# Optimization experiments

Hardware: AMD Instinct MI355X
Metric: run time of the kernel (lower is better)

## Reference

```python
import jax, jax.numpy as jnp
import numpy as np

TASK_NUM = 100000
WORKER_NUM = 500
FEATURE_SIZE = 512
CLASS_NUM = 10
ANSWER_NUM = 1000000
HIDDEN = 128
NUM_NODES = TASK_NUM + WORKER_NUM


def setup_inputs() -> dict:
    key = jax.random.key(0)
    ks = jax.random.split(key, 10)
    task_ids = jax.random.randint(ks[0], (ANSWER_NUM,), 0, TASK_NUM, dtype=jnp.int32)
    worker_ids = jax.random.randint(ks[1], (ANSWER_NUM,), 0, WORKER_NUM, dtype=jnp.int32)
    label_ids = jax.random.randint(ks[2], (ANSWER_NUM,), 0, CLASS_NUM, dtype=jnp.int32)
    answers = jnp.stack([task_ids, worker_ids, label_ids], axis=1)  # [A,3]
    return {
        "task_feature": jax.random.normal(ks[3], (TASK_NUM, FEATURE_SIZE), jnp.float32),
        "answers": answers,
        "worker_feature": jax.random.normal(ks[4], (WORKER_NUM, HIDDEN), jnp.float32),
        "W_efc": jax.random.normal(ks[5], (FEATURE_SIZE, HIDDEN), jnp.float32) * 0.05,
        "b_efc": jnp.zeros((HIDDEN,), jnp.float32),
        "W_mean": jax.random.normal(ks[6], (HIDDEN, CLASS_NUM), jnp.float32) * 0.05,
        "b_mean": jnp.zeros((CLASS_NUM,), jnp.float32),
        "W_log_std": jax.random.normal(ks[7], (HIDDEN, CLASS_NUM), jnp.float32) * 0.05,
        "b_log_std": jnp.zeros((CLASS_NUM,), jnp.float32),
        "eps": jax.random.normal(ks[8], (NUM_NODES, CLASS_NUM), jnp.float32),
    }


def _gcn_edges(task_ids, worker_ids):
    # Bipartite edges doubled to be symmetric, plus self-loops (renorm trick).
    row0 = task_ids
    col0 = worker_ids + TASK_NUM
    self_idx = jnp.arange(NUM_NODES, dtype=jnp.int32)
    row = jnp.concatenate([row0, col0, self_idx])
    col = jnp.concatenate([col0, row0, self_idx])
    deg = jax.ops.segment_sum(jnp.ones_like(row, dtype=jnp.float32), row,
                              num_segments=NUM_NODES)
    dinv = jax.lax.rsqrt(deg)  # deg >= 1 thanks to self-loops
    w = dinv[row] * dinv[col]  # [E]
    return row, col, w, row0, col0


def _gcn(x, kernel, bias, row, col, w):
    h = x @ kernel                                   # [N, C]
    msg = h[col] * w[:, None]                        # gather + scale
    return jax.ops.segment_sum(msg, row, num_segments=NUM_NODES) + bias


def reference(task_feature, answers, worker_feature, W_efc, b_efc,
              W_mean, b_mean, W_log_std, b_log_std, eps):
    row, col, w, row0, col0 = _gcn_edges(answers[:, 0], answers[:, 1])
    tf_h = jax.nn.relu(task_feature @ W_efc + b_efc)           # [T, 128]
    x = jnp.concatenate([tf_h, worker_feature], axis=0)        # [N, 128]
    mean = _gcn(x, W_mean, b_mean, row, col, w)                # [N, C]
    log_std = _gcn(x, W_log_std, b_log_std, row, col, w)       # [N, C]
    z = mean + (eps * 0.01) * jnp.exp(log_std)                 # reparam, stddev 0.01
    crowd_out = z[row0] * z[col0]                              # [A, C]
    return crowd_out, mean, log_std
```

## Files before the change

kernel.cpp:

```cpp
#include <hip/hip_runtime.h>

#define T_NUM   100000
#define W_NUM   500
#define N_NODES 100500
#define A_NUM   1000000
#define FEAT    512
#define HID     128
#define CLS     10

#define CSR_STRIDE  40
#define CSRT_STRIDE 2432
#define BM          64
#define HPAD        136
#define NRANGE      8
#define TRNG        (T_NUM / NRANGE)
#define WRNG        64
#define CHUNK       2048
#define NCHUNK      ((A_NUM + CHUNK - 1) / CHUNK)
#define BLD_CAP     64

typedef short bf16x8 __attribute__((ext_vector_type(8)));
typedef float f32x4  __attribute__((ext_vector_type(4)));

__device__ __forceinline__ unsigned cvtpk(float lo, float hi) {
    unsigned r;
    asm("v_cvt_pk_bf16_f32 %0, %1, %2" : "=v"(r) : "v"(lo), "v"(hi));
    return r;
}
__device__ __forceinline__ unsigned short f2bf1(float x) {
    return (unsigned short)cvtpk(x, x);
}

__global__ __launch_bounds__(256) void k_build(
        const int* __restrict__ answers, int* __restrict__ cnt,
        int* __restrict__ wcur, int* __restrict__ tick,
        unsigned short* __restrict__ csrW, int* __restrict__ csrT) {
    __shared__ int lcnt[WRNG];
    __shared__ int llist[WRNG * BLD_CAP];
    __shared__ int s_chunk;

    int xcc;
    asm volatile("s_getreg_b32 %0, hwreg(HW_REG_XCC_ID)" : "=s"(xcc));
    const int r   = xcc & (NRANGE - 1);
    const int tlo = r * TRNG, thi = tlo + TRNG;
    const int wlo = r * WRNG;

    for (int i = threadIdx.x; i < WRNG; i += 256) lcnt[i] = 0;

    for (;;) {
        __syncthreads();
        if (threadIdx.x == 0) s_chunk = atomicAdd(&tick[r * 16], 1);
        __syncthreads();
        const int c = s_chunk;
        if (c >= NCHUNK) break;
        const int base = c * CHUNK;
        const int end  = (base + CHUNK < A_NUM) ? base + CHUNK : A_NUM;
        for (int a = base + threadIdx.x; a < end; a += 256) {
            int t = __builtin_nontemporal_load(answers + a * 3);
            int w = __builtin_nontemporal_load(answers + a * 3 + 1);
            if (t >= tlo && t < thi) {
                int p = atomicAdd(&cnt[t], 1);
                if (p < CSR_STRIDE) csrW[(size_t)t * CSR_STRIDE + p] = (unsigned short)w;
            }
            int wr = w - wlo;
            if (wr >= 0 && wr < WRNG && w < W_NUM) {
                int s = atomicAdd(&lcnt[wr], 1);
                if (s < BLD_CAP) llist[wr * BLD_CAP + s] = t;
                else {
                    int q = atomicAdd(&wcur[w * 16], 1);
                    if (q < CSRT_STRIDE) csrT[(size_t)w * CSRT_STRIDE + q] = t;
                }
            }
        }
    }
    __syncthreads();

    for (int wr = threadIdx.x; wr < WRNG; wr += 256) {
        int w = wlo + wr;
        if (w >= W_NUM) continue;
        int c = lcnt[wr];
        if (c > BLD_CAP) c = BLD_CAP;
        if (c == 0) continue;
        int qb = atomicAdd(&wcur[w * 16], c);
        int* dst = csrT + (size_t)w * CSRT_STRIDE;
        for (int j = 0; j < c; j++) {
            int q = qb + j;
            if (q < CSRT_STRIDE) dst[q] = llist[wr * BLD_CAP + j];
        }
    }
}

__global__ void k_prepw(const float* __restrict__ W, unsigned short* __restrict__ Wt,
                        unsigned short* __restrict__ B2t,
                        const float* __restrict__ WF,
                        const float* __restrict__ Wm, const float* __restrict__ Wl,
                        const int* __restrict__ wcur,
                        float* __restrict__ g) {
    int bid = blockIdx.x;
    if (bid < HID) {
        int c = bid;
        for (int k = threadIdx.x; k < FEAT; k += blockDim.x)
            Wt[(size_t)c * FEAT + k] = f2bf1(W[(size_t)k * HID + c]);
    } else if (bid == HID) {
        for (int i = threadIdx.x; i < 32 * HID; i += blockDim.x) {
            int c = i / HID, k = i % HID;
            float v = 0.f;
            if (c < 10)                 v = Wm[k * CLS + c];
            else if (c >= 16 && c < 26) v = Wl[k * CLS + (c - 16)];
            B2t[i] = f2bf1(v);
        }
    } else {
        int idx = (bid - HID - 1) * blockDim.x + threadIdx.x;
        if (idx >= W_NUM * 20) return;
        int w = idx / 20, oc = idx % 20;
        const float* Wc = (oc < 10) ? (Wm + oc) : (Wl + (oc - 10));
        const float* x  = WF + (size_t)w * HID;
        float s = 0.f;
        #pragma unroll 8
        for (int k = 0; k < HID; k++) s = fmaf(x[k], Wc[k * CLS], s);
        float gi = rsqrtf((float)(wcur[w * 16] + 1)) * s;
        g[(size_t)(T_NUM + w) * 20 + oc] = gi;
    }
}

__global__ __launch_bounds__(256, 7) void k_gemm_mfma(
        const float* __restrict__ A, const unsigned short* __restrict__ Wt,
        const float* __restrict__ bias, const unsigned short* __restrict__ B2t,
        const int* __restrict__ cnt, float* __restrict__ g) {
    __shared__ __align__(16) char smem[17408];

    const int tid  = threadIdx.x;
    const int lane = tid & 63;
    const int wv   = tid >> 6;
    const int l15  = lane & 15;
    const int lkg  = lane >> 4;
    const int row  = blockIdx.x * BM + wv * 16 + l15;
    const int rowc = row < T_NUM ? row : T_NUM - 1;
    const float* aptr = A + (size_t)rowc * FEAT + lkg * 8;

    const int scol  = tid >> 1;
    const int shalf = tid & 1;
    const int sswz  = (scol & 7) << 4;
    const int sb0   = (scol * 64 + shalf * 32) ^ sswz;
    const int sb1   = (scol * 64 + shalf * 32 + 16) ^ sswz;
    const unsigned short* sptr = Wt + (size_t)scol * FEAT + shalf * 16;

    const int rswz = (l15 & 7) << 4;

    f32x4 acc[8];
    #pragma unroll
    for (int nt = 0; nt < 8; nt++) acc[nt] = (f32x4){0.f, 0.f, 0.f, 0.f};

    union LU { int4 i; bf16x8 h; };
    union PK { unsigned u[4]; bf16x8 h; };

    float4 ca0 = *(const float4*)(aptr);
    float4 ca1 = *(const float4*)(aptr + 4);
    *(int4*)(smem + sb0) = *(const int4*)(sptr);
    *(int4*)(smem + sb1) = *(const int4*)(sptr + 8);
    __syncthreads();

    for (int ks = 0; ks < 16; ks++) {
        const int k0 = ks * 32;
        float4 na0, na1;
        if (ks < 15) {
            na0 = *(const float4*)(aptr + k0 + 32);
            na1 = *(const float4*)(aptr + k0 + 36);
            char* nb = smem + (((ks + 1) & 1) << 13);
            *(int4*)(nb + sb0) = *(const int4*)(sptr + k0 + 32);
            *(int4*)(nb + sb1) = *(const int4*)(sptr + k0 + 40);
        }
        PK pk;
        pk.u[0] = cvtpk(ca0.x, ca0.y);
        pk.u[1] = cvtpk(ca0.z, ca0.w);
        pk.u[2] = cvtpk(ca1.x, ca1.y);
        pk.u[3] = cvtpk(ca1.z, ca1.w);
        const char* bb = smem + ((ks & 1) << 13);
        #pragma unroll
        for (int nt = 0; nt < 8; nt++) {
            const int boff = ((nt * 16 + l15) * 64 + lkg * 16) ^ rswz;
            LU bu; bu.i = *(const int4*)(bb + boff);
            acc[nt] = __builtin_amdgcn_mfma_f32_16x16x32_bf16(pk.h, bu.h, acc[nt], 0, 0, 0);
        }
        ca0 = na0; ca1 = na1;
        __syncthreads();
    }

    unsigned short* hw = (unsigned short*)smem + wv * 16 * HPAD;
    #pragma unroll
    for (int nt = 0; nt < 8; nt++) {
        float bv = bias[nt * 16 + l15];
        #pragma unroll
        for (int r = 0; r < 4; r++) {
            float h = fmaxf(acc[nt][r] + bv, 0.f);
            hw[(lkg * 4 + r) * HPAD + nt * 16 + l15] = f2bf1(h);
        }
    }

    f32x4 acc2[2];
    acc2[0] = (f32x4){0.f, 0.f, 0.f, 0.f};
    acc2[1] = (f32x4){0.f, 0.f, 0.f, 0.f};
    #pragma unroll
    for (int s = 0; s < 4; s++) {
        LU a2;
        a2.i = *(const int4*)(hw + l15 * HPAD + s * 32 + lkg * 8);
        #pragma unroll
        for (int j = 0; j < 2; j++) {
            LU b2;
            b2.i = *(const int4*)(B2t + (size_t)(j * 16 + l15) * HID + s * 32 + lkg * 8);
            acc2[j] = __builtin_amdgcn_mfma_f32_16x16x32_bf16(a2.h, b2.h, acc2[j], 0, 0, 0);
        }
    }

    if (l15 < 10) {
        #pragma unroll
        for (int r = 0; r < 4; r++) {
            int node = blockIdx.x * BM + wv * 16 + lkg * 4 + r;
            if (node < T_NUM) {
                float di = rsqrtf((float)(cnt[node] + 1));
                g[(size_t)node * 20 + l15]      = di * acc2[0][r];
                g[(size_t)node * 20 + 10 + l15] = di * acc2[1][r];
            }
        }
    }
}

__global__ __launch_bounds__(256) void k_wacc(
        const int* __restrict__ csrT, const int* __restrict__ wcur,
        const float* __restrict__ g,
        const float* __restrict__ b_mean, const float* __restrict__ b_ls,
        const float* __restrict__ eps,
        float* __restrict__ out_mean, float* __restrict__ out_ls,
        float* __restrict__ z) {
    const int w    = blockIdx.x;
    const int tid  = threadIdx.x;
    const int lane = tid & 63;
    const int wv   = tid >> 6;

    int len = wcur[w * 16];
    int lim = len < CSRT_STRIDE ? len : CSRT_STRIDE;
    const int* lst = csrT + (size_t)w * CSRT_STRIDE;

    float a[20];
    #pragma unroll
    for (int c = 0; c < 20; c++) a[c] = 0.f;

    for (int e = tid; e < lim; e += 256) {
        int t = lst[e];
        const float4* gr = (const float4*)(g + (size_t)t * 20);
        float4 v0 = gr[0], v1 = gr[1], v2 = gr[2], v3 = gr[3], v4 = gr[4];
        a[0] += v0.x; a[1] += v0.y; a[2] += v0.z; a[3] += v0.w;
        a[4] += v1.x; a[5] += v1.y; a[6] += v1.z; a[7] += v1.w;
        a[8] += v2.x; a[9] += v2.y; a[10] += v2.z; a[11] += v2.w;
        a[12] += v3.x; a[13] += v3.y; a[14] += v3.z; a[15] += v3.w;
        a[16] += v4.x; a[17] += v4.y; a[18] += v4.z; a[19] += v4.w;
    }

    #pragma unroll
    for (int off = 32; off; off >>= 1) {
        #pragma unroll
        for (int c = 0; c < 20; c++) a[c] += __shfl_down(a[c], off, 64);
    }

    __shared__ float wpart[4][20];
    __shared__ float fin[20];
    if (lane == 0) {
        #pragma unroll
        for (int c = 0; c < 20; c++) wpart[wv][c] = a[c];
    }
    __syncthreads();

    const int node = T_NUM + w;
    if (tid < 20) {
        float s = wpart[0][tid] + wpart[1][tid] + wpart[2][tid] + wpart[3][tid];
        float di = rsqrtf((float)(len + 1));
        float gv = g[(size_t)node * 20 + tid];
        if (tid < 10) {
            float m = fmaf(di, s + gv, b_mean[tid]);
            out_mean[(size_t)node * CLS + tid] = m;
            fin[tid] = m;
        } else {
            int c = tid - 10;
            float l = fmaf(di, s + gv, b_ls[c]);
            out_ls[(size_t)node * CLS + c] = l;
            fin[tid] = l;
        }
    }
    __syncthreads();
    if (tid < 10) {
        float m = fin[tid], l = fin[tid + 10];
        z[(size_t)node * CLS + tid] =
            fmaf(eps[(size_t)node * CLS + tid] * 0.01f, expf(l), m);
    }
}

__global__ __launch_bounds__(256) void k_gather_task(
        const int* __restrict__ cnt, const unsigned short* __restrict__ csrW,
        const float* __restrict__ g,
        const float* __restrict__ b_mean, const float* __restrict__ b_ls,
        const float* __restrict__ eps,
        float* __restrict__ out_mean, float* __restrict__ out_ls,
        float* __restrict__ z) {
    __shared__ float gw[W_NUM * 21];
    for (int i = threadIdx.x; i < W_NUM * 20; i += blockDim.x)
        gw[(i / 20) * 21 + (i % 20)] = g[(size_t)T_NUM * 20 + i];
    __syncthreads();

    int t = blockIdx.x * blockDim.x + threadIdx.x;
    if (t >= T_NUM) return;

    int len = cnt[t];
    int lim = len < CSR_STRIDE ? len : CSR_STRIDE;
    const unsigned short* lst = csrW + (size_t)t * CSR_STRIDE;
    float am[10], al[10];
    #pragma unroll
    for (int c = 0; c < 10; c++) { am[c] = 0.f; al[c] = 0.f; }

    for (int e = 0; e < lim; e++) {
        const float* gg = &gw[lst[e] * 21];
        #pragma unroll
        for (int c = 0; c < 10; c++) {
            am[c] += gg[c];
            al[c] += gg[10 + c];
        }
    }

    float di = rsqrtf((float)(len + 1));
    union { float4 v[5]; float f[20]; } grow;
    const float4* gr = (const float4*)(g + (size_t)t * 20);
    #pragma unroll
    for (int c = 0; c < 5; c++) grow.v[c] = gr[c];

    const float2* ep2 = (const float2*)(eps + (size_t)t * CLS);
    float2* om2 = (float2*)(out_mean + (size_t)t * CLS);
    float2* ol2 = (float2*)(out_ls + (size_t)t * CLS);
    float2* z2  = (float2*)(z + (size_t)t * CLS);
    #pragma unroll
    for (int c = 0; c < 5; c++) {
        float2 ev = ep2[c];
        float m0 = fmaf(di, am[2 * c] + grow.f[2 * c], b_mean[2 * c]);
        float m1 = fmaf(di, am[2 * c + 1] + grow.f[2 * c + 1], b_mean[2 * c + 1]);
        float l0 = fmaf(di, al[2 * c] + grow.f[10 + 2 * c], b_ls[2 * c]);
        float l1 = fmaf(di, al[2 * c + 1] + grow.f[10 + 2 * c + 1], b_ls[2 * c + 1]);
        om2[c] = make_float2(m0, m1);
        ol2[c] = make_float2(l0, l1);
        z2[c]  = make_float2(fmaf(ev.x * 0.01f, expf(l0), m0),
                             fmaf(ev.y * 0.01f, expf(l1), m1));
    }
}

__global__ void k_crowd(const int* __restrict__ answers, const float* __restrict__ z,
                        float* __restrict__ out) {
    int i = blockIdx.x * blockDim.x + threadIdx.x;
    if (i >= A_NUM * 5) return;
    int a = i / 5, c2 = i % 5;
    int t = answers[a * 3 + 0];
    int w = answers[a * 3 + 1];
    float2 x = *(const float2*)(z + (size_t)t * CLS + c2 * 2);
    float2 y = *(const float2*)(z + (size_t)(T_NUM + w) * CLS + c2 * 2);
    *(float2*)(out + (size_t)i * 2) = make_float2(x.x * y.x, x.y * y.y);
}

extern "C" void kernel_launch(void* const* d_in, const int* in_sizes, int n_in,
                              void* d_out, int out_size, void* d_ws, size_t ws_size,
                              hipStream_t stream) {
    const float* task_feature   = (const float*)d_in[0];
    const int*   answers        = (const int*)d_in[1];
    const float* worker_feature = (const float*)d_in[2];
    const float* W_efc          = (const float*)d_in[3];
    const float* b_efc          = (const float*)d_in[4];
    const float* W_mean         = (const float*)d_in[5];
    const float* b_mean         = (const float*)d_in[6];
    const float* W_ls           = (const float*)d_in[7];
    const float* b_ls           = (const float*)d_in[8];
    const float* eps            = (const float*)d_in[9];

    float* out       = (float*)d_out;
    float* out_crowd = out;
    float* out_mean  = out + (size_t)A_NUM * CLS;
    float* out_ls    = out_mean + (size_t)N_NODES * CLS;

    char* ws = (char*)d_ws;
    int* cnt              = (int*)ws;
    int* wcur             = (int*)(ws + 402432);
    int* tick             = (int*)(ws + 434432);
    unsigned short* csrW  = (unsigned short*)(ws + 434944);
    unsigned short* Wt    = (unsigned short*)(ws + 8434944);
    unsigned short* B2t   = (unsigned short*)(ws + 8566016);
    int* csrT             = (int*)(ws + 8574208);
    float* g              = (float*)(ws + 13438208);
    float* z              = (float*)(ws + 21478208);

    hipMemsetAsync(ws, 0, 434944, stream);

    k_build<<<2048, 256, 0, stream>>>(answers, cnt, wcur, tick, csrW, csrT);
    k_prepw<<<HID + 1 + (W_NUM * 20 + 255) / 256, 256, 0, stream>>>(
        W_efc, Wt, B2t, worker_feature, W_mean, W_ls, wcur, g);
    k_gemm_mfma<<<(T_NUM + BM - 1) / BM, 256, 0, stream>>>(
        task_feature, Wt, b_efc, B2t, cnt, g);
    k_wacc<<<W_NUM, 256, 0, stream>>>(csrT, wcur, g, b_mean, b_ls, eps,
                                      out_mean, out_ls, z);
    k_gather_task<<<(T_NUM + 255) / 256, 256, 0, stream>>>(
        cnt, csrW, g, b_mean, b_ls, eps, out_mean, out_ls, z);
    k_crowd<<<(A_NUM * 5 + 255) / 256, 256, 0, stream>>>(answers, z, out_crowd);
}
```

Before: 208.1 us.

## Fuse CSR build into the GEMM launch so the two stages overlap

Merges the adjacency build and the task-feature MFMA GEMM into one launch, with extra blocks past the GEMM grid running the build. Each build block walks all eight node ranges, starting from the one tied to its XCC. Because the GEMM no longer waits for degrees, it writes unscaled projections. The degree normalization moves to the consumers: a per-edge rsqrt(cnt) in the worker accumulation, and a self-row scale in the task gather. The worker projection becomes its own kernel launched after the build. This is meant to hide the atomic-heavy build behind the bandwidth-bound GEMM and to remove a launch boundary, at the cost of an extra random cnt load per edge and contention between the two workloads.

```diff
diff --git a/kernel.cpp b/kernel.cpp
--- a/kernel.cpp
+++ b/kernel.cpp
@@ -18,6 +18,8 @@
 #define CHUNK       2048
 #define NCHUNK      ((A_NUM + CHUNK - 1) / CHUNK)
 #define BLD_CAP     64
+#define GEMM_BLKS   ((T_NUM + BM - 1) / BM)
+#define BUILD_BLKS  1024
 
 typedef short bf16x8 __attribute__((ext_vector_type(8)));
 typedef float f32x4  __attribute__((ext_vector_type(4)));
@@ -31,77 +33,15 @@
     return (unsigned short)cvtpk(x, x);
 }
 
-__global__ __launch_bounds__(256) void k_build(
-        const int* __restrict__ answers, int* __restrict__ cnt,
-        int* __restrict__ wcur, int* __restrict__ tick,
-        unsigned short* __restrict__ csrW, int* __restrict__ csrT) {
-    __shared__ int lcnt[WRNG];
-    __shared__ int llist[WRNG * BLD_CAP];
-    __shared__ int s_chunk;
-
-    int xcc;
-    asm volatile("s_getreg_b32 %0, hwreg(HW_REG_XCC_ID)" : "=s"(xcc));
-    const int r   = xcc & (NRANGE - 1);
-    const int tlo = r * TRNG, thi = tlo + TRNG;
-    const int wlo = r * WRNG;
-
-    for (int i = threadIdx.x; i < WRNG; i += 256) lcnt[i] = 0;
-
-    for (;;) {
-        __syncthreads();
-        if (threadIdx.x == 0) s_chunk = atomicAdd(&tick[r * 16], 1);
-        __syncthreads();
-        const int c = s_chunk;
-        if (c >= NCHUNK) break;
-        const int base = c * CHUNK;
-        const int end  = (base + CHUNK < A_NUM) ? base + CHUNK : A_NUM;
-        for (int a = base + threadIdx.x; a < end; a += 256) {
-            int t = __builtin_nontemporal_load(answers + a * 3);
-            int w = __builtin_nontemporal_load(answers + a * 3 + 1);
-            if (t >= tlo && t < thi) {
-                int p = atomicAdd(&cnt[t], 1);
-                if (p < CSR_STRIDE) csrW[(size_t)t * CSR_STRIDE + p] = (unsigned short)w;
-            }
-            int wr = w - wlo;
-            if (wr >= 0 && wr < WRNG && w < W_NUM) {
-                int s = atomicAdd(&lcnt[wr], 1);
-                if (s < BLD_CAP) llist[wr * BLD_CAP + s] = t;
-                else {
-                    int q = atomicAdd(&wcur[w * 16], 1);
-                    if (q < CSRT_STRIDE) csrT[(size_t)w * CSRT_STRIDE + q] = t;
-                }
-            }
-        }
-    }
-    __syncthreads();
-
-    for (int wr = threadIdx.x; wr < WRNG; wr += 256) {
-        int w = wlo + wr;
-        if (w >= W_NUM) continue;
-        int c = lcnt[wr];
-        if (c > BLD_CAP) c = BLD_CAP;
-        if (c == 0) continue;
-        int qb = atomicAdd(&wcur[w * 16], c);
-        int* dst = csrT + (size_t)w * CSRT_STRIDE;
-        for (int j = 0; j < c; j++) {
-            int q = qb + j;
-            if (q < CSRT_STRIDE) dst[q] = llist[wr * BLD_CAP + j];
-        }
-    }
-}
-
 __global__ void k_prepw(const float* __restrict__ W, unsigned short* __restrict__ Wt,
                         unsigned short* __restrict__ B2t,
-                        const float* __restrict__ WF,
-                        const float* __restrict__ Wm, const float* __restrict__ Wl,
-                        const int* __restrict__ wcur,
-                        float* __restrict__ g) {
+                        const float* __restrict__ Wm, const float* __restrict__ Wl) {
     int bid = blockIdx.x;
     if (bid < HID) {
         int c = bid;
         for (int k = threadIdx.x; k < FEAT; k += blockDim.x)
             Wt[(size_t)c * FEAT + k] = f2bf1(W[(size_t)k * HID + c]);
-    } else if (bid == HID) {
+    } else {
         for (int i = threadIdx.x; i < 32 * HID; i += blockDim.x) {
             int c = i / HID, k = i % HID;
             float v = 0.f;
@@ -109,27 +49,81 @@
             else if (c >= 16 && c < 26) v = Wl[k * CLS + (c - 16)];
             B2t[i] = f2bf1(v);
         }
-    } else {
-        int idx = (bid - HID - 1) * blockDim.x + threadIdx.x;
-        if (idx >= W_NUM * 20) return;
-        int w = idx / 20, oc = idx % 20;
-        const float* Wc = (oc < 10) ? (Wm + oc) : (Wl + (oc - 10));
-        const float* x  = WF + (size_t)w * HID;
-        float s = 0.f;
-        #pragma unroll 8
-        for (int k = 0; k < HID; k++) s = fmaf(x[k], Wc[k * CLS], s);
-        float gi = rsqrtf((float)(wcur[w * 16] + 1)) * s;
-        g[(size_t)(T_NUM + w) * 20 + oc] = gi;
-    }
-}
-
-__global__ __launch_bounds__(256, 7) void k_gemm_mfma(
+    }
+}
+
+__global__ __launch_bounds__(256, 7) void k_fused(
         const float* __restrict__ A, const unsigned short* __restrict__ Wt,
         const float* __restrict__ bias, const unsigned short* __restrict__ B2t,
-        const int* __restrict__ cnt, float* __restrict__ g) {
-    __shared__ __align__(16) char smem[17408];
-
-    const int tid  = threadIdx.x;
+        float* __restrict__ g,
+        const int* __restrict__ answers, int* __restrict__ cnt,
+        int* __restrict__ wcur, int* __restrict__ tick,
+        unsigned short* __restrict__ csrW, int* __restrict__ csrT) {
+    __shared__ __align__(16) char smem[17664];
+    const int tid = threadIdx.x;
+
+    if (blockIdx.x >= GEMM_BLKS) {
+        int* lcnt    = (int*)smem;
+        int* llist   = (int*)(smem + 256);
+        int* s_chunk = (int*)(smem + 16640);
+
+        int xcc;
+        asm volatile("s_getreg_b32 %0, hwreg(HW_REG_XCC_ID)" : "=s"(xcc));
+        const int r0 = xcc & (NRANGE - 1);
+
+        for (int rr = 0; rr < NRANGE; rr++) {
+            const int re  = (r0 + rr) & (NRANGE - 1);
+            const int tlo = re * TRNG, thi = tlo + TRNG;
+            const int wlo = re * WRNG;
+
+            for (int i = tid; i < WRNG; i += 256) lcnt[i] = 0;
+
+            for (;;) {
+                __syncthreads();
+                if (tid == 0) *s_chunk = atomicAdd(&tick[re * 16], 1);
+                __syncthreads();
+                const int c = *s_chunk;
+                if (c >= NCHUNK) break;
+                const int base = c * CHUNK;
+                const int end  = (base + CHUNK < A_NUM) ? base + CHUNK : A_NUM;
+                for (int a = base + tid; a < end; a += 256) {
+                    int t = __builtin_nontemporal_load(answers + a * 3);
+                    int w = __builtin_nontemporal_load(answers + a * 3 + 1);
+                    if (t >= tlo && t < thi) {
+                        int p = atomicAdd(&cnt[t], 1);
+                        if (p < CSR_STRIDE)
+                            csrW[(size_t)t * CSR_STRIDE + p] = (unsigned short)w;
+                    }
+                    int wr = w - wlo;
+                    if (wr >= 0 && wr < WRNG && w < W_NUM) {
+                        int s = atomicAdd(&lcnt[wr], 1);
+                        if (s < BLD_CAP) llist[wr * BLD_CAP + s] = t;
+                        else {
+                            int q = atomicAdd(&wcur[w * 16], 1);
+                            if (q < CSRT_STRIDE)
+                                csrT[(size_t)w * CSRT_STRIDE + q] = t;
+                        }
+                    }
+                }
+            }
+            for (int wr = tid; wr < WRNG; wr += 256) {
+                int w = wlo + wr;
+                if (w >= W_NUM) continue;
+                int c = lcnt[wr];
+                if (c > BLD_CAP) c = BLD_CAP;
+                if (c == 0) continue;
+                int qb = atomicAdd(&wcur[w * 16], c);
+                int* dst = csrT + (size_t)w * CSRT_STRIDE;
+                for (int j = 0; j < c; j++) {
+                    int q = qb + j;
+                    if (q < CSRT_STRIDE) dst[q] = llist[wr * BLD_CAP + j];
+                }
+            }
+            __syncthreads();
+        }
+        return;
+    }
+
     const int lane = tid & 63;
     const int wv   = tid >> 6;
     const int l15  = lane & 15;
@@ -217,17 +211,31 @@
         for (int r = 0; r < 4; r++) {
             int node = blockIdx.x * BM + wv * 16 + lkg * 4 + r;
             if (node < T_NUM) {
-                float di = rsqrtf((float)(cnt[node] + 1));
-                g[(size_t)node * 20 + l15]      = di * acc2[0][r];
-                g[(size_t)node * 20 + 10 + l15] = di * acc2[1][r];
+                g[(size_t)node * 20 + l15]      = acc2[0][r];
+                g[(size_t)node * 20 + 10 + l15] = acc2[1][r];
             }
         }
     }
+}
+
+__global__ void k_wproj(const float* __restrict__ WF,
+                        const float* __restrict__ Wm, const float* __restrict__ Wl,
+                        const int* __restrict__ wcur, float* __restrict__ g) {
+    int idx = blockIdx.x * blockDim.x + threadIdx.x;
+    if (idx >= W_NUM * 20) return;
+    int w = idx / 20, oc = idx % 20;
+    const float* Wc = (oc < 10) ? (Wm + oc) : (Wl + (oc - 10));
+    const float* x  = WF + (size_t)w * HID;
+    float s = 0.f;
+    #pragma unroll 8
+    for (int k = 0; k < HID; k++) s = fmaf(x[k], Wc[k * CLS], s);
+    float gi = rsqrtf((float)(wcur[w * 16] + 1)) * s;
+    g[(size_t)(T_NUM + w) * 20 + oc] = gi;
 }
 
 __global__ __launch_bounds__(256) void k_wacc(
         const int* __restrict__ csrT, const int* __restrict__ wcur,
-        const float* __restrict__ g,
+        const int* __restrict__ cnt, const float* __restrict__ g,
         const float* __restrict__ b_mean, const float* __restrict__ b_ls,
         const float* __restrict__ eps,
         float* __restrict__ out_mean, float* __restrict__ out_ls,
@@ -247,13 +255,14 @@
 
     for (int e = tid; e < lim; e += 256) {
         int t = lst[e];
+        float dit = rsqrtf((float)(cnt[t] + 1));
         const float4* gr = (const float4*)(g + (size_t)t * 20);
         float4 v0 = gr[0], v1 = gr[1], v2 = gr[2], v3 = gr[3], v4 = gr[4];
-        a[0] += v0.x; a[1] += v0.y; a[2] += v0.z; a[3] += v0.w;
-        a[4] += v1.x; a[5] += v1.y; a[6] += v1.z; a[7] += v1.w;
-        a[8] += v2.x; a[9] += v2.y; a[10] += v2.z; a[11] += v2.w;
-        a[12] += v3.x; a[13] += v3.y; a[14] += v3.z; a[15] += v3.w;
-        a[16] += v4.x; a[17] += v4.y; a[18] += v4.z; a[19] += v4.w;
+        a[0] += dit * v0.x; a[1] += dit * v0.y; a[2] += dit * v0.z; a[3] += dit * v0.w;
+        a[4] += dit * v1.x; a[5] += dit * v1.y; a[6] += dit * v1.z; a[7] += dit * v1.w;
+        a[8] += dit * v2.x; a[9] += dit * v2.y; a[10] += dit * v2.z; a[11] += dit * v2.w;
+        a[12] += dit * v3.x; a[13] += dit * v3.y; a[14] += dit * v3.z; a[15] += dit * v3.w;
+        a[16] += dit * v4.x; a[17] += dit * v4.y; a[18] += dit * v4.z; a[19] += dit * v4.w;
     }
 
     #pragma unroll
@@ -330,6 +339,8 @@
     const float4* gr = (const float4*)(g + (size_t)t * 20);
     #pragma unroll
     for (int c = 0; c < 5; c++) grow.v[c] = gr[c];
+    #pragma unroll
+    for (int k = 0; k < 20; k++) grow.f[k] *= di;
 
     const float2* ep2 = (const float2*)(eps + (size_t)t * CLS);
     float2* om2 = (float2*)(out_mean + (size_t)t * CLS);
@@ -393,12 +404,13 @@
 
     hipMemsetAsync(ws, 0, 434944, stream);
 
-    k_build<<<2048, 256, 0, stream>>>(answers, cnt, wcur, tick, csrW, csrT);
-    k_prepw<<<HID + 1 + (W_NUM * 20 + 255) / 256, 256, 0, stream>>>(
-        W_efc, Wt, B2t, worker_feature, W_mean, W_ls, wcur, g);
-    k_gemm_mfma<<<(T_NUM + BM - 1) / BM, 256, 0, stream>>>(
-        task_feature, Wt, b_efc, B2t, cnt, g);
-    k_wacc<<<W_NUM, 256, 0, stream>>>(csrT, wcur, g, b_mean, b_ls, eps,
+    k_prepw<<<HID + 1, 256, 0, stream>>>(W_efc, Wt, B2t, W_mean, W_ls);
+    k_fused<<<GEMM_BLKS + BUILD_BLKS, 256, 0, stream>>>(
+        task_feature, Wt, b_efc, B2t, g,
+        answers, cnt, wcur, tick, csrW, csrT);
+    k_wproj<<<(W_NUM * 20 + 255) / 256, 256, 0, stream>>>(
+        worker_feature, W_mean, W_ls, wcur, g);
+    k_wacc<<<W_NUM, 256, 0, stream>>>(csrT, wcur, cnt, g, b_mean, b_ls, eps,
                                       out_mean, out_ls, z);
     k_gather_task<<<(T_NUM + 255) / 256, 256, 0, stream>>>(
         cnt, csrW, g, b_mean, b_ls, eps, out_mean, out_ls, z);
```

Result: slower. 212.5 us (+2.1%).
